# Kernel optimization log

Measured on AMD Instinct MI355X. Metric: run time of the kernel, lower is better.

The kernel has to match this reference:

```python
import jax, jax.numpy as jnp
import numpy as np
from jax import lax

B, L, D_MODEL = 2, 2048, 1024
D_INNER, D_STATE, DT_RANK, D_CONV = 2048, 16, 64, 4


def setup_inputs() -> dict:
    key = jax.random.key(0)
    ks = jax.random.split(key, 10)
    s = 0.02
    A_log = jnp.log(jnp.broadcast_to(jnp.arange(1, D_STATE + 1, dtype=jnp.float32), (D_INNER, D_STATE)))
    return {
        "x": jax.random.normal(ks[0], (B, L, D_MODEL), jnp.float32),
        "in_proj_w": jax.random.normal(ks[1], (2 * D_INNER, D_MODEL), jnp.float32) * s,
        "conv_w": jax.random.normal(ks[2], (D_INNER, 1, D_CONV), jnp.float32) * s,
        "conv_b": jax.random.normal(ks[3], (D_INNER,), jnp.float32) * s,
        "x_proj_w": jax.random.normal(ks[4], (DT_RANK + 2 * D_STATE, D_INNER), jnp.float32) * s,
        "dt_proj_w": jax.random.normal(ks[5], (D_INNER, DT_RANK), jnp.float32) * s,
        "dt_proj_b": jax.random.normal(ks[6], (D_INNER,), jnp.float32) * s,
        "A_log": A_log,
        "D": jnp.ones((D_INNER,), jnp.float32),
        "out_proj_w": jax.random.normal(ks[7], (D_MODEL, D_INNER), jnp.float32) * s,
    }


def _silu(v):
    return v * jax.nn.sigmoid(v)


def _mamba_forward(x, in_proj_w, conv_w, conv_b, x_proj_w, dt_proj_w, dt_proj_b, A_log, D, out_proj_w):
    b, l, _ = x.shape
    xr = jnp.einsum('bld,ed->ble', x, in_proj_w)          # (b, l, 2*d_inner)
    xs, res = jnp.split(xr, 2, axis=-1)
    # causal depthwise conv over time
    xc = jnp.transpose(xs, (0, 2, 1))                     # (b, d_inner, l)
    xc = lax.conv_general_dilated(
        xc, conv_w, window_strides=(1,), padding=[(D_CONV - 1, 0)],
        feature_group_count=D_INNER,
        dimension_numbers=('NCH', 'OIH', 'NCH')) + conv_b[None, :, None]
    u = _silu(jnp.transpose(xc, (0, 2, 1)))               # (b, l, d_inner)
    # SSM parameters
    A = -jnp.exp(A_log)                                   # (d_inner, d_state)
    x_dbl = jnp.einsum('bld,ed->ble', u, x_proj_w)        # (b, l, dt_rank + 2*d_state)
    dt, Bm, Cm = jnp.split(x_dbl, [DT_RANK, DT_RANK + D_STATE], axis=-1)
    delta = jax.nn.softplus(jnp.einsum('blr,dr->bld', dt, dt_proj_w) + dt_proj_b)
    # discretize
    deltaA = jnp.exp(jnp.einsum('bld,dn->bldn', delta, A))        # (b, l, d_inner, d_state)
    deltaBu = jnp.einsum('bld,bln,bld->bldn', delta, Bm, u)       # (b, l, d_inner, d_state)
    # sequential selective scan over time
    def step(h, inp):
        dA, dBu, c = inp
        h = dA * h + dBu                                  # (b, d_inner, d_state)
        y = jnp.einsum('bdn,bn->bd', h, c)
        return h, y
    xs_scan = (jnp.transpose(deltaA, (1, 0, 2, 3)),
               jnp.transpose(deltaBu, (1, 0, 2, 3)),
               jnp.transpose(Cm, (1, 0, 2)))
    h0 = jnp.zeros((b, D_INNER, D_STATE), u.dtype)
    _, ys = lax.scan(step, h0, xs_scan)                   # (l, b, d_inner)
    y = jnp.transpose(ys, (1, 0, 2)) + u * D              # skip connection
    y = y * _silu(res)                                    # gate
    return jnp.einsum('bld,ed->ble', y, out_proj_w)       # (b, l, d_model)


def reference(x, in_proj_w, conv_w, conv_b, x_proj_w, dt_proj_w, dt_proj_b, A_log, D, out_proj_w):
    return _mamba_forward(x, in_proj_w, conv_w, conv_b, x_proj_w, dt_proj_w, dt_proj_b, A_log, D, out_proj_w)
```

## Files before the change

kernel.cpp:

```cpp
#include <hip/hip_runtime.h>
#include <hip/hip_bf16.h>
#include <math.h>

#define B_SZ 2
#define L_SZ 2048
#define DMODEL 1024
#define DINNER 2048
#define DSTATE 16
#define DTRANK 64
#define M_ROWS (B_SZ * L_SZ)

#define CH 32
#define CLEN (L_SZ / CH)
#define CPB 64

#define KSPLIT 8
#define KC (DINNER / KSPLIT)

typedef short shortx8 __attribute__((ext_vector_type(8)));
typedef float floatx4 __attribute__((ext_vector_type(4)));
typedef float floatx16 __attribute__((ext_vector_type(16)));

__device__ __forceinline__ float softplusf(float x) {
    return fmaxf(x, 0.f) + log1pf(expf(-fabsf(x)));
}
__device__ __forceinline__ float siluf(float x) {
    return x * (1.f / (1.f + expf(-x)));
}

__device__ __forceinline__ void async_ld16(const void* g, void* l) {
    __builtin_amdgcn_global_load_lds(
        (__attribute__((address_space(1))) void*)(unsigned long long)g,
        (__attribute__((address_space(3))) void*)(unsigned int)(unsigned long long)l,
        16, 0, 0);
}


template <int ROWS, int KSRC>
__global__ __launch_bounds__(256) void split3_kernel(
    const float* __restrict__ src, unsigned short* __restrict__ dst)
{
    constexpr int SEGT = KSRC / 64;
    int i = blockIdx.x * 256 + threadIdx.x;
    int row = i & (ROWS - 1);
    int k8s = i / ROWS;
    const float* s = src + (size_t)row * KSRC + k8s * 8;
    float4 v0 = *(const float4*)s;
    float4 v1 = *(const float4*)(s + 4);
    float vs[8] = {v0.x, v0.y, v0.z, v0.w, v1.x, v1.y, v1.z, v1.w};
    unsigned short hsv[8], lsv[8];
#pragma unroll
    for (int j = 0; j < 8; ++j) {
        __hip_bfloat16 h = __float2bfloat16(vs[j]);
        __hip_bfloat16 l = __float2bfloat16(vs[j] - __bfloat162float(h));
        hsv[j] = *(unsigned short*)&h;
        lsv[j] = *(unsigned short*)&l;
    }
    int tloc = k8s >> 3;
    int sh = (k8s >> 2) & 1;
    int k8l = k8s & 3;
    size_t off = ((size_t)(row >> 8) * 4 * SEGT + tloc * 2 + sh) * 8192
               + (size_t)(k8l * 256 + (row & 255)) * 8;
    *(shortx8*)&dst[off] = *(shortx8*)hsv;
    *(shortx8*)&dst[off + (size_t)2 * SEGT * 8192] = *(shortx8*)lsv;
}

template <int LDSRC>
__global__ __launch_bounds__(256) void split2k_kernel(
    const float* __restrict__ src, unsigned short* __restrict__ dst)
{
    int i = blockIdx.x * 256 + threadIdx.x;
    int m = i >> 6, k = i & 63;
    float a = src[(size_t)m * LDSRC + k];
    __hip_bfloat16 h = __float2bfloat16(a);
    __hip_bfloat16 l = __float2bfloat16(a - __bfloat162float(h));
    unsigned short* row = dst + (size_t)m * 128;
    row[k] = *(unsigned short*)&h;
    row[64 + k] = *(unsigned short*)&l;
}

template <int KT, int SEGT, int NB, int LDC>
__global__ __launch_bounds__(512, 2) void gemm_8ph(
    const unsigned short* __restrict__ Ap,
    const unsigned short* __restrict__ Bp,
    float* __restrict__ C)
{
    __shared__ unsigned short lds[65536];

    const int tid = threadIdx.x;
    const int lane = tid & 63;
    const int w = tid >> 6;
    const int wm = w >> 2, wn = w & 3;
    const int l15 = lane & 15, l4 = lane >> 4;

    int id = blockIdx.x;
    id = (id & 7) * 32 + (id >> 3);
    const int bm = id / NB;
    const int bn = id % NB;

    const unsigned short* ga = Ap + (size_t)bm * 4 * SEGT * 8192;
    const unsigned short* gb = Bp + (size_t)bn * 4 * SEGT * 8192;

    const int rA = (l4 * 256 + wm * 128 + l15) * 8;
    const int rB = (l4 * 256 + wn * 64 + l15) * 8;

    floatx4 acc[8][4] = {};
    shortx8 bfr[4];

    auto STAGE = [&](int vt, int ab, int s) {
        int Tv = vt < KT ? vt : KT - 1;
        int Tm = ab ? (Tv >= SEGT ? Tv - SEGT : Tv)
                    : (Tv >= 2 * SEGT ? Tv - 2 * SEGT : Tv);
        const unsigned short* src = (ab ? gb : ga) + ((size_t)Tm * 2 + s) * 8192 + tid * 8;
        unsigned short* dst = (unsigned short*)lds + (vt & 1) * 32768 + ab * 16384 + s * 8192 + tid * 8;
        async_ld16(src, dst);
        async_ld16(src + 4096, dst + 4096);
    };

#define MFMA16(MH)                                                                             \
    acc[(MH)*4+0][0] = __builtin_amdgcn_mfma_f32_16x16x32_bf16(af0, bfr[0], acc[(MH)*4+0][0], 0,0,0); \
    acc[(MH)*4+0][1] = __builtin_amdgcn_mfma_f32_16x16x32_bf16(af0, bfr[1], acc[(MH)*4+0][1], 0,0,0); \
    acc[(MH)*4+0][2] = __builtin_amdgcn_mfma_f32_16x16x32_bf16(af0, bfr[2], acc[(MH)*4+0][2], 0,0,0); \
    acc[(MH)*4+0][3] = __builtin_amdgcn_mfma_f32_16x16x32_bf16(af0, bfr[3], acc[(MH)*4+0][3], 0,0,0); \
    acc[(MH)*4+1][0] = __builtin_amdgcn_mfma_f32_16x16x32_bf16(af1, bfr[0], acc[(MH)*4+1][0], 0,0,0); \
    acc[(MH)*4+1][1] = __builtin_amdgcn_mfma_f32_16x16x32_bf16(af1, bfr[1], acc[(MH)*4+1][1], 0,0,0); \
    acc[(MH)*4+1][2] = __builtin_amdgcn_mfma_f32_16x16x32_bf16(af1, bfr[2], acc[(MH)*4+1][2], 0,0,0); \
    acc[(MH)*4+1][3] = __builtin_amdgcn_mfma_f32_16x16x32_bf16(af1, bfr[3], acc[(MH)*4+1][3], 0,0,0); \
    acc[(MH)*4+2][0] = __builtin_amdgcn_mfma_f32_16x16x32_bf16(af2, bfr[0], acc[(MH)*4+2][0], 0,0,0); \
    acc[(MH)*4+2][1] = __builtin_amdgcn_mfma_f32_16x16x32_bf16(af2, bfr[1], acc[(MH)*4+2][1], 0,0,0); \
    acc[(MH)*4+2][2] = __builtin_amdgcn_mfma_f32_16x16x32_bf16(af2, bfr[2], acc[(MH)*4+2][2], 0,0,0); \
    acc[(MH)*4+2][3] = __builtin_amdgcn_mfma_f32_16x16x32_bf16(af2, bfr[3], acc[(MH)*4+2][3], 0,0,0); \
    acc[(MH)*4+3][0] = __builtin_amdgcn_mfma_f32_16x16x32_bf16(af3, bfr[0], acc[(MH)*4+3][0], 0,0,0); \
    acc[(MH)*4+3][1] = __builtin_amdgcn_mfma_f32_16x16x32_bf16(af3, bfr[1], acc[(MH)*4+3][1], 0,0,0); \
    acc[(MH)*4+3][2] = __builtin_amdgcn_mfma_f32_16x16x32_bf16(af3, bfr[2], acc[(MH)*4+3][2], 0,0,0); \
    acc[(MH)*4+3][3] = __builtin_amdgcn_mfma_f32_16x16x32_bf16(af3, bfr[3], acc[(MH)*4+3][3], 0,0,0);

#define PHASE(SLOT, S, MH, SVT, SAB, SS, VM)                                   \
    {                                                                          \
        const unsigned short* Ab = &lds[(SLOT)*32768 + (S)*8192] + rA;         \
        shortx8 af0 = *(const shortx8*)&Ab[((MH)*4 + 0) * 128];                \
        shortx8 af1 = *(const shortx8*)&Ab[((MH)*4 + 1) * 128];                \
        shortx8 af2 = *(const shortx8*)&Ab[((MH)*4 + 2) * 128];                \
        shortx8 af3 = *(const shortx8*)&Ab[((MH)*4 + 3) * 128];                \
        if ((MH) == 0) {                                                       \
            const unsigned short* Bb = &lds[(SLOT)*32768 + 16384 + (S)*8192] + rB; \
            bfr[0] = *(const shortx8*)&Bb[0];                                  \
            bfr[1] = *(const shortx8*)&Bb[128];                                \
            bfr[2] = *(const shortx8*)&Bb[256];                                \
            bfr[3] = *(const shortx8*)&Bb[384];                                \
        }                                                                      \
        STAGE(SVT, SAB, SS);                                                   \
        __builtin_amdgcn_s_barrier();                                          \
        asm volatile("s_waitcnt lgkmcnt(0)" ::: "memory");                     \
        __builtin_amdgcn_s_setprio(1);                                         \
        MFMA16(MH)                                                             \
        __builtin_amdgcn_s_setprio(0);                                         \
        if (VM) { asm volatile("s_waitcnt vmcnt(4)" ::: "memory"); }           \
        __builtin_amdgcn_s_barrier();                                          \
    }

    STAGE(0, 0, 0); STAGE(0, 1, 0); STAGE(0, 0, 1); STAGE(0, 1, 1);
    STAGE(1, 0, 0); STAGE(1, 1, 0);
    asm volatile("s_waitcnt vmcnt(4)" ::: "memory");
    __builtin_amdgcn_s_barrier();

#pragma unroll 1
    for (int i = 0; i < KT / 2; ++i) {
        const int t2 = 2 * i;
        PHASE(0, 0, 0, t2 + 1, 0, 1, 0)
        PHASE(0, 0, 1, t2 + 1, 1, 1, 0)
        PHASE(0, 1, 0, t2 + 2, 0, 0, 0)
        PHASE(0, 1, 1, t2 + 2, 1, 0, 1)
        PHASE(1, 0, 0, t2 + 2, 0, 1, 0)
        PHASE(1, 0, 1, t2 + 2, 1, 1, 0)
        PHASE(1, 1, 0, t2 + 3, 0, 0, 0)
        PHASE(1, 1, 1, t2 + 3, 1, 0, 1)
    }

#undef PHASE
#undef MFMA16

    const int c0 = bn * 256 + wn * 64;
    const int r0 = bm * 256 + wm * 128;
#pragma unroll
    for (int fi = 0; fi < 8; ++fi) {
#pragma unroll
        for (int fj = 0; fj < 4; ++fj) {
            int col = c0 + fj * 16 + l15;
            int rowb = r0 + fi * 16 + l4 * 4;
#pragma unroll
            for (int ri = 0; ri < 4; ++ri)
                C[(size_t)(rowb + ri) * LDC + col] = acc[fi][fj][ri];
        }
    }
}

template <int BN, int KP>
__global__ __launch_bounds__(256) void gemm_bf16_nt(
    const unsigned short* __restrict__ A,
    const unsigned short* __restrict__ Bm,
    float* __restrict__ C, int ldc)
{
    constexpr int TN32 = BN / 64;
    __shared__ unsigned short As[2 * 8192];
    __shared__ unsigned short Bs[2 * BN * 64];

    const int tid = threadIdx.x;
    const int w = tid >> 6;
    const int lane = tid & 63;
    const int wm = w >> 1, wn = w & 1;
    const int m0 = blockIdx.y * 128;
    const int n0 = blockIdx.x * BN;

    const int r4 = lane >> 2;
    const int csw = (lane & 3) ^ ((r4 >> 1) & 3);
    const int gk = csw * 8;
    const int l31 = lane & 31;
    const int khalf = lane >> 5;
    const int rsw = (l31 >> 1) & 3;

    floatx16 acc[2][TN32] = {};

    for (int k0 = 0; k0 < KP; k0 += 64) {
#pragma unroll
        for (int seg = 0; seg < 2; ++seg) {
            const unsigned short* Asrc = A + seg * KP;
            const unsigned short* Bsrc = Bm + seg * KP;
#pragma unroll
            for (int t = 0; t < 2; ++t) {
#pragma unroll
                for (int jj = 0; jj < 2; ++jj) {
                    int j = w + jj * 4;
                    async_ld16(Asrc + (size_t)(m0 + j * 16 + r4) * (2 * KP) + k0 + t * 32 + gk,
                               &As[seg * 8192 + t * 4096 + j * 512]);
                }
#pragma unroll
                for (int jj = 0; jj < BN / 64; ++jj) {
                    int j = w + jj * 4;
                    async_ld16(Bsrc + (size_t)(n0 + j * 16 + r4) * (2 * KP) + k0 + t * 32 + gk,
                               &Bs[seg * BN * 64 + t * BN * 32 + j * 512]);
                }
            }
        }
        __syncthreads();

#pragma unroll
        for (int t = 0; t < 2; ++t) {
#pragma unroll
            for (int kk = 0; kk < 2; ++kk) {
                const int pos = ((kk * 2 + khalf) ^ rsw) << 3;
                shortx8 ah[2], al[2], bh[TN32], bl[TN32];
#pragma unroll
                for (int i = 0; i < 2; ++i) {
                    int row = wm * 64 + i * 32 + l31;
                    ah[i] = *(const shortx8*)&As[t * 4096 + row * 32 + pos];
                    al[i] = *(const shortx8*)&As[8192 + t * 4096 + row * 32 + pos];
                }
#pragma unroll
                for (int j = 0; j < TN32; ++j) {
                    int col = wn * (BN / 2) + j * 32 + l31;
                    bh[j] = *(const shortx8*)&Bs[t * BN * 32 + col * 32 + pos];
                    bl[j] = *(const shortx8*)&Bs[BN * 64 + t * BN * 32 + col * 32 + pos];
                }
#pragma unroll
                for (int i = 0; i < 2; ++i)
#pragma unroll
                    for (int j = 0; j < TN32; ++j) {
                        acc[i][j] = __builtin_amdgcn_mfma_f32_32x32x16_bf16(ah[i], bh[j], acc[i][j], 0, 0, 0);
                        acc[i][j] = __builtin_amdgcn_mfma_f32_32x32x16_bf16(ah[i], bl[j], acc[i][j], 0, 0, 0);
                        acc[i][j] = __builtin_amdgcn_mfma_f32_32x32x16_bf16(al[i], bh[j], acc[i][j], 0, 0, 0);
                    }
            }
        }
        __syncthreads();
    }

#pragma unroll
    for (int i = 0; i < 2; ++i) {
#pragma unroll
        for (int j = 0; j < TN32; ++j) {
            int col = n0 + wn * (BN / 2) + j * 32 + l31;
#pragma unroll
            for (int r = 0; r < 16; ++r) {
                int row = m0 + wm * 64 + i * 32 + (r & 3) + 8 * (r >> 2) + 4 * khalf;
                C[(size_t)row * ldc + col] = acc[i][j][r];
            }
        }
    }
}

template <int BN, int KP>
__global__ __launch_bounds__(256) void gemm_bf16_sp(
    const unsigned short* __restrict__ A,
    const unsigned short* __restrict__ Bm,
    float* __restrict__ C, int ldc, const float* __restrict__ bias)
{
    constexpr int TN32 = BN / 64;
    __shared__ unsigned short As[2 * 8192];
    __shared__ unsigned short Bs[2 * BN * 64];

    const int tid = threadIdx.x;
    const int w = tid >> 6;
    const int lane = tid & 63;
    const int wm = w >> 1, wn = w & 1;
    const int m0 = blockIdx.y * 128;
    const int n0 = blockIdx.x * BN;

    const int r4 = lane >> 2;
    const int csw = (lane & 3) ^ ((r4 >> 1) & 3);
    const int gk = csw * 8;
    const int l31 = lane & 31;
    const int khalf = lane >> 5;
    const int rsw = (l31 >> 1) & 3;

    floatx16 acc[2][TN32] = {};

    for (int k0 = 0; k0 < KP; k0 += 64) {
#pragma unroll
        for (int seg = 0; seg < 2; ++seg) {
            const unsigned short* Asrc = A + seg * KP;
            const unsigned short* Bsrc = Bm + seg * KP;
#pragma unroll
            for (int t = 0; t < 2; ++t) {
#pragma unroll
                for (int jj = 0; jj < 2; ++jj) {
                    int j = w + jj * 4;
                    async_ld16(Asrc + (size_t)(m0 + j * 16 + r4) * (2 * KP) + k0 + t * 32 + gk,
                               &As[seg * 8192 + t * 4096 + j * 512]);
                }
#pragma unroll
                for (int jj = 0; jj < BN / 64; ++jj) {
                    int j = w + jj * 4;
                    async_ld16(Bsrc + (size_t)(n0 + j * 16 + r4) * (2 * KP) + k0 + t * 32 + gk,
                               &Bs[seg * BN * 64 + t * BN * 32 + j * 512]);
                }
            }
        }
        __syncthreads();

#pragma unroll
        for (int t = 0; t < 2; ++t) {
#pragma unroll
            for (int kk = 0; kk < 2; ++kk) {
                const int pos = ((kk * 2 + khalf) ^ rsw) << 3;
                shortx8 ah[2], al[2], bh[TN32], bl[TN32];
#pragma unroll
                for (int i = 0; i < 2; ++i) {
                    int row = wm * 64 + i * 32 + l31;
                    ah[i] = *(const shortx8*)&As[t * 4096 + row * 32 + pos];
                    al[i] = *(const shortx8*)&As[8192 + t * 4096 + row * 32 + pos];
                }
#pragma unroll
                for (int j = 0; j < TN32; ++j) {
                    int col = wn * (BN / 2) + j * 32 + l31;
                    bh[j] = *(const shortx8*)&Bs[t * BN * 32 + col * 32 + pos];
                    bl[j] = *(const shortx8*)&Bs[BN * 64 + t * BN * 32 + col * 32 + pos];
                }
#pragma unroll
                for (int i = 0; i < 2; ++i)
#pragma unroll
                    for (int j = 0; j < TN32; ++j) {
                        acc[i][j] = __builtin_amdgcn_mfma_f32_32x32x16_bf16(ah[i], bh[j], acc[i][j], 0, 0, 0);
                        acc[i][j] = __builtin_amdgcn_mfma_f32_32x32x16_bf16(ah[i], bl[j], acc[i][j], 0, 0, 0);
                        acc[i][j] = __builtin_amdgcn_mfma_f32_32x32x16_bf16(al[i], bh[j], acc[i][j], 0, 0, 0);
                    }
            }
        }
        __syncthreads();
    }

#pragma unroll
    for (int i = 0; i < 2; ++i) {
#pragma unroll
        for (int j = 0; j < TN32; ++j) {
            int col = n0 + wn * (BN / 2) + j * 32 + l31;
            float bz = bias[col];
#pragma unroll
            for (int r = 0; r < 16; ++r) {
                int row = m0 + wm * 64 + i * 32 + (r & 3) + 8 * (r >> 2) + 4 * khalf;
                C[(size_t)row * ldc + col] = softplusf(acc[i][j][r] + bz);
            }
        }
    }
}

__global__ __launch_bounds__(256) void split2_kernel(
    const float* __restrict__ src, unsigned short* __restrict__ dst, int K)
{
    int i = blockIdx.x * 256 + threadIdx.x;
    int m = i / K;
    int k = i - m * K;
    float a = src[i];
    __hip_bfloat16 h = __float2bfloat16(a);
    __hip_bfloat16 l = __float2bfloat16(a - __bfloat162float(h));
    unsigned short* row = dst + (size_t)m * 2 * K;
    row[k] = *(unsigned short*)&h;
    row[K + k] = *(unsigned short*)&l;
}

__global__ __launch_bounds__(256) void xproj_splitk(
    const float* __restrict__ u, const float* __restrict__ Wx,
    float* __restrict__ Cp)
{
    __shared__ float As[64][68];
    __shared__ float Bs[64][100];

    const int tid = threadIdx.x;
    const int ks = blockIdx.x;
    const int m0 = blockIdx.y * 64;
    const int tx = tid & 15;
    const int ty = tid >> 4;

    float acc[4][6] = {};

    for (int k0 = ks * KC; k0 < (ks + 1) * KC; k0 += 64) {
        for (int idx = tid * 4; idx < 64 * 64; idx += 1024) {
            int row = idx >> 6, kk = idx & 63;
            float4 v = *(const float4*)&u[(size_t)(m0 + row) * DINNER + k0 + kk];
            As[kk + 0][row] = v.x;
            As[kk + 1][row] = v.y;
            As[kk + 2][row] = v.z;
            As[kk + 3][row] = v.w;
        }
        for (int idx = tid * 4; idx < 96 * 64; idx += 1024) {
            int row = idx >> 6, kk = idx & 63;
            float4 v = *(const float4*)&Wx[(size_t)row * DINNER + k0 + kk];
            Bs[kk + 0][row] = v.x;
            Bs[kk + 1][row] = v.y;
            Bs[kk + 2][row] = v.z;
            Bs[kk + 3][row] = v.w;
        }
        __syncthreads();

#pragma unroll 8
        for (int k = 0; k < 64; ++k) {
            float a[4], b[6];
#pragma unroll
            for (int i = 0; i < 4; ++i) a[i] = As[k][ty * 4 + i];
#pragma unroll
            for (int j = 0; j < 6; ++j) b[j] = Bs[k][tx * 6 + j];
#pragma unroll
            for (int i = 0; i < 4; ++i)
#pragma unroll
                for (int j = 0; j < 6; ++j) acc[i][j] = fmaf(a[i], b[j], acc[i][j]);
        }
        __syncthreads();
    }

    float* outp = Cp + ((size_t)ks * M_ROWS + m0) * 96;
#pragma unroll
    for (int i = 0; i < 4; ++i)
#pragma unroll
        for (int j = 0; j < 6; ++j)
            outp[(ty * 4 + i) * 96 + tx * 6 + j] = acc[i][j];
}

__global__ __launch_bounds__(256) void xproj_reduce(
    const float* __restrict__ Cp, float* __restrict__ xdbl)
{
    int i = blockIdx.x * 256 + threadIdx.x;
    float s = 0.f;
#pragma unroll
    for (int c = 0; c < KSPLIT; ++c)
        s += Cp[(size_t)c * M_ROWS * 96 + i];
    xdbl[i] = s;
}

__global__ __launch_bounds__(256) void conv_silu_v4(
    const float* __restrict__ xz, const float* __restrict__ cw,
    const float* __restrict__ cb, float* __restrict__ u)
{
    int i = blockIdx.x * 256 + threadIdx.x;
    int dq = (i & 511) << 2;
    int bl = i >> 9;
    int b = bl >> 11;
    int l = bl & 2047;

    float4 W0 = *(const float4*)&cw[(dq + 0) * 4];
    float4 W1 = *(const float4*)&cw[(dq + 1) * 4];
    float4 W2 = *(const float4*)&cw[(dq + 2) * 4];
    float4 W3 = *(const float4*)&cw[(dq + 3) * 4];
    float4 acc = *(const float4*)&cb[dq];

#pragma unroll
    for (int k = 0; k < 4; ++k) {
        int ls = l + k - 3;
        if (ls >= 0) {
            float4 v = *(const float4*)&xz[((size_t)(b << 11) + ls) * 4096 + dq];
            acc.x = fmaf(v.x, ((const float*)&W0)[k], acc.x);
            acc.y = fmaf(v.y, ((const float*)&W1)[k], acc.y);
            acc.z = fmaf(v.z, ((const float*)&W2)[k], acc.z);
            acc.w = fmaf(v.w, ((const float*)&W3)[k], acc.w);
        }
    }
    float4 r = make_float4(siluf(acc.x), siluf(acc.y), siluf(acc.z), siluf(acc.w));
    *(float4*)&u[(size_t)bl * DINNER + dq] = r;
}

template <bool PASS3>
__global__ __launch_bounds__(256) void scan_chunk(
    const float* __restrict__ dbuf, const float* __restrict__ ubuf,
    const float* __restrict__ xdbl, const float* __restrict__ A_log,
    const float* __restrict__ Dv,
    float* __restrict__ Pbuf, float* __restrict__ Sbuf,
    const float* __restrict__ xz, unsigned short* __restrict__ y2)
{
    __shared__ float sd[16][CPB];
    __shared__ float su[16][CPB];
    __shared__ float sB[16][DSTATE];
    __shared__ float sC[16][DSTATE];

    const int tid = threadIdx.x;
    const int c    = blockIdx.x % CH;
    const int dblk = (blockIdx.x / CH) % (DINNER / CPB);
    const int b    = blockIdx.x / (CH * (DINNER / CPB));
    const int d0 = dblk * CPB;
    const int dg = tid >> 2;
    const int q  = tid & 3;
    const int d  = d0 + dg;
    const size_t base_bl = (size_t)b * L_SZ + (size_t)c * CLEN;

    float Ac[4], h[4];
    float sdl = 0.f;
#pragma unroll
    for (int j = 0; j < 4; ++j)
        Ac[j] = -expf(A_log[d * DSTATE + 4 * q + j]);
    const size_t psoff = (((size_t)b * CH + c) * DINNER + d0) * DSTATE + (size_t)tid * 4;
    if (PASS3) {
        float4 h0 = *(const float4*)&Sbuf[psoff];
        h[0] = h0.x; h[1] = h0.y; h[2] = h0.z; h[3] = h0.w;
    } else {
        h[0] = h[1] = h[2] = h[3] = 0.f;
    }
    const float Dd = PASS3 ? Dv[d] : 0.f;

    const int ls = tid >> 4;
    const int g4 = (tid & 15) * 4;
    const int ln = tid & 15;

    float4 r_d = *(const float4*)&dbuf[(base_bl + ls) * DINNER + d0 + g4];
    float4 r_u = *(const float4*)&ubuf[(base_bl + ls) * DINNER + d0 + g4];
    float r_B = xdbl[(base_bl + ls) * 96 + 64 + ln];
    float r_C = xdbl[(base_bl + ls) * 96 + 80 + ln];

    for (int l0 = 0; l0 < CLEN; l0 += 16) {
        __syncthreads();
        *(float4*)&sd[ls][g4] = r_d;
        *(float4*)&su[ls][g4] = r_u;
        sB[ls][ln] = r_B;
        sC[ls][ln] = r_C;
        __syncthreads();

        if (l0 + 16 < CLEN) {
            r_d = *(const float4*)&dbuf[(base_bl + l0 + 16 + ls) * DINNER + d0 + g4];
            r_u = *(const float4*)&ubuf[(base_bl + l0 + 16 + ls) * DINNER + d0 + g4];
            r_B = xdbl[(base_bl + l0 + 16 + ls) * 96 + 64 + ln];
            r_C = xdbl[(base_bl + l0 + 16 + ls) * 96 + 80 + ln];
        }

#pragma unroll
        for (int s = 0; s < 16; ++s) {
            float dl = sd[s][dg];
            float ul = su[s][dg];
            float4 Bv = *(float4*)&sB[s][4 * q];
            float dbu = dl * ul;
            float dA0 = expf(dl * Ac[0]);
            float dA1 = expf(dl * Ac[1]);
            float dA2 = expf(dl * Ac[2]);
            float dA3 = expf(dl * Ac[3]);
            h[0] = fmaf(dA0, h[0], dbu * Bv.x);
            h[1] = fmaf(dA1, h[1], dbu * Bv.y);
            h[2] = fmaf(dA2, h[2], dbu * Bv.z);
            h[3] = fmaf(dA3, h[3], dbu * Bv.w);
            if (!PASS3) {
                sdl += dl;
            } else {
                float4 Cv = *(float4*)&sC[s][4 * q];
                float y = h[0] * Cv.x + h[1] * Cv.y + h[2] * Cv.z + h[3] * Cv.w;
                y += __shfl_xor(y, 1);
                y += __shfl_xor(y, 2);
                if (q == 0) su[s][dg] = fmaf(ul, Dd, y);
            }
        }

        if (PASS3) {
            __syncthreads();
            size_t row = base_bl + l0 + ls;
            float4 yv = *(float4*)&su[ls][g4];
            float4 rv = *(const float4*)&xz[row * 4096 + 2048 + d0 + g4];
            float a0 = yv.x * siluf(rv.x);
            float a1 = yv.y * siluf(rv.y);
            float a2 = yv.z * siluf(rv.z);
            float a3 = yv.w * siluf(rv.w);
            __hip_bfloat16 h0 = __float2bfloat16(a0), h1 = __float2bfloat16(a1);
            __hip_bfloat16 h2 = __float2bfloat16(a2), h3 = __float2bfloat16(a3);
            __hip_bfloat16 l0b = __float2bfloat16(a0 - __bfloat162float(h0));
            __hip_bfloat16 l1b = __float2bfloat16(a1 - __bfloat162float(h1));
            __hip_bfloat16 l2b = __float2bfloat16(a2 - __bfloat162float(h2));
            __hip_bfloat16 l3b = __float2bfloat16(a3 - __bfloat162float(h3));
            ushort4 hv = make_ushort4(*(unsigned short*)&h0, *(unsigned short*)&h1,
                                      *(unsigned short*)&h2, *(unsigned short*)&h3);
            ushort4 lv = make_ushort4(*(unsigned short*)&l0b, *(unsigned short*)&l1b,
                                      *(unsigned short*)&l2b, *(unsigned short*)&l3b);
            unsigned short* yrow = y2 + row * 2 * DINNER + d0 + g4;
            *(ushort4*)&yrow[0] = hv;
            *(ushort4*)&yrow[DINNER] = lv;
        }
    }

    if (!PASS3) {
        *(float4*)&Pbuf[psoff] = make_float4(expf(Ac[0] * sdl), expf(Ac[1] * sdl),
                                             expf(Ac[2] * sdl), expf(Ac[3] * sdl));
        *(float4*)&Sbuf[psoff] = make_float4(h[0], h[1], h[2], h[3]);
    }
}

__global__ __launch_bounds__(256) void scan_combine(
    const float* __restrict__ Pbuf, float* __restrict__ Sbuf)
{
    int t = blockIdx.x * 256 + threadIdx.x;
    int b = t >> 15;
    int rem = t & 32767;
    size_t base = (size_t)b * CH * DINNER * DSTATE + rem;
    float H = 0.f;
#pragma unroll 4
    for (int c = 0; c < CH; ++c) {
        size_t off = base + (size_t)c * DINNER * DSTATE;
        float S = Sbuf[off];
        float P = Pbuf[off];
        Sbuf[off] = H;
        H = fmaf(P, H, S);
    }
}

extern "C" void kernel_launch(void* const* d_in, const int* in_sizes, int n_in,
                              void* d_out, int out_size, void* d_ws, size_t ws_size,
                              hipStream_t stream)
{
    const float* x          = (const float*)d_in[0];
    const float* in_proj_w  = (const float*)d_in[1];
    const float* conv_w     = (const float*)d_in[2];
    const float* conv_b     = (const float*)d_in[3];
    const float* x_proj_w   = (const float*)d_in[4];
    const float* dt_proj_w  = (const float*)d_in[5];
    const float* dt_proj_b  = (const float*)d_in[6];
    const float* A_log      = (const float*)d_in[7];
    const float* Dv         = (const float*)d_in[8];
    const float* out_proj_w = (const float*)d_in[9];
    float* out = (float*)d_out;

    char* w = (char*)d_ws;
    float* xz   = (float*)(w);
    float* u    = (float*)(w + 67108864);
    float* dbuf = (float*)(w + 100663296);
    float* xdbl = (float*)(w + 134217728);
    float* Pbuf = (float*)(w + 135790592);
    float* Sbuf = (float*)(w + 144179200);
    unsigned short* y2  = (unsigned short*)(w + 152567808);
    unsigned short* w2b = (unsigned short*)(w + 135790592);
    float* Cp = (float*)(w + 152567808);
    unsigned short* dt2  = (unsigned short*)(w + 152567808);
    unsigned short* wdt2 = (unsigned short*)(w + 152567808 + 1048576);
    unsigned short* x2p  = (unsigned short*)(w + 67108864);
    unsigned short* w2ap = (unsigned short*)(w + 100663296);

    split3_kernel<4096, 1024><<<2048, 256, 0, stream>>>(x, x2p);
    split3_kernel<4096, 1024><<<2048, 256, 0, stream>>>(in_proj_w, w2ap);
    gemm_8ph<48, 16, 16, 4096><<<256, 512, 0, stream>>>(x2p, w2ap, xz);
    conv_silu_v4<<<(M_ROWS * 512) / 256, 256, 0, stream>>>(xz, conv_w, conv_b, u);
    {
        dim3 g(KSPLIT, M_ROWS / 64);
        xproj_splitk<<<g, 256, 0, stream>>>(u, x_proj_w, Cp);
        xproj_reduce<<<(M_ROWS * 96) / 256, 256, 0, stream>>>(Cp, xdbl);
    }
    {
        split2k_kernel<96><<<1024, 256, 0, stream>>>(xdbl, dt2);
        split2k_kernel<64><<<512, 256, 0, stream>>>(dt_proj_w, wdt2);
        dim3 g(DINNER / 64, M_ROWS / 128);
        gemm_bf16_sp<64, 64><<<g, 256, 0, stream>>>(dt2, wdt2, dbuf, DINNER, dt_proj_b);
    }
    {
        const int nblk = B_SZ * (DINNER / CPB) * CH;
        scan_chunk<false><<<nblk, 256, 0, stream>>>(dbuf, u, xdbl, A_log, Dv, Pbuf, Sbuf, nullptr, nullptr);
        scan_combine<<<B_SZ * DINNER * DSTATE / 256, 256, 0, stream>>>(Pbuf, Sbuf);
        scan_chunk<true><<<nblk, 256, 0, stream>>>(dbuf, u, xdbl, A_log, Dv, nullptr, Sbuf, xz, y2);
    }
    split2_kernel<<<(DMODEL * DINNER) / 256, 256, 0, stream>>>(out_proj_w, w2b, DINNER);
    {
        dim3 g(1024 / 64, M_ROWS / 128);
        gemm_bf16_nt<64, 2048><<<g, 256, 0, stream>>>(y2, w2b, out, 1024);
    }
}
```

Baseline: 510.0 us.

## Use 128x128 tiles with 8 waves for out_proj GEMM; coarsen split3 threads

The out_proj bf16x3 GEMM now uses 128x128 output tiles with 512 threads (8 waves, each computing 64x32) in place of 128x64 tiles with 4 waves. This halves the number of times the A operand is reloaded across N tiles and raises the MFMA work per block. The grid shrinks to 8x32 = 256 blocks, which may underfill the CUs. Separately, the split3 conversion kernel has each thread process 32 consecutive floats instead of 8, using a quarter of the blocks. This cuts index math and improves read contiguity.

Measured after the change: 500.4 us. About the same (-1.9%).

```diff
diff --git a/kernel.cpp b/kernel.cpp
--- a/kernel.cpp
+++ b/kernel.cpp
@@ -43,26 +43,29 @@
     constexpr int SEGT = KSRC / 64;
     int i = blockIdx.x * 256 + threadIdx.x;
     int row = i & (ROWS - 1);
-    int k8s = i / ROWS;
-    const float* s = src + (size_t)row * KSRC + k8s * 8;
-    float4 v0 = *(const float4*)s;
-    float4 v1 = *(const float4*)(s + 4);
-    float vs[8] = {v0.x, v0.y, v0.z, v0.w, v1.x, v1.y, v1.z, v1.w};
-    unsigned short hsv[8], lsv[8];
-#pragma unroll
-    for (int j = 0; j < 8; ++j) {
-        __hip_bfloat16 h = __float2bfloat16(vs[j]);
-        __hip_bfloat16 l = __float2bfloat16(vs[j] - __bfloat162float(h));
-        hsv[j] = *(unsigned short*)&h;
-        lsv[j] = *(unsigned short*)&l;
-    }
-    int tloc = k8s >> 3;
-    int sh = (k8s >> 2) & 1;
-    int k8l = k8s & 3;
-    size_t off = ((size_t)(row >> 8) * 4 * SEGT + tloc * 2 + sh) * 8192
-               + (size_t)(k8l * 256 + (row & 255)) * 8;
-    *(shortx8*)&dst[off] = *(shortx8*)hsv;
-    *(shortx8*)&dst[off + (size_t)2 * SEGT * 8192] = *(shortx8*)lsv;
+    int g = i / ROWS;
+    const float* s = src + (size_t)row * KSRC + g * 32;
+    int tloc = g >> 1;
+    int sh = g & 1;
+    size_t base = ((size_t)(row >> 8) * 4 * SEGT + tloc * 2 + sh) * 8192
+                + (size_t)(row & 255) * 8;
+#pragma unroll
+    for (int q = 0; q < 4; ++q) {
+        float4 v0 = *(const float4*)(s + q * 8);
+        float4 v1 = *(const float4*)(s + q * 8 + 4);
+        float fs[8] = {v0.x, v0.y, v0.z, v0.w, v1.x, v1.y, v1.z, v1.w};
+        shortx8 hv, lv;
+#pragma unroll
+        for (int j = 0; j < 8; ++j) {
+            __hip_bfloat16 h = __float2bfloat16(fs[j]);
+            __hip_bfloat16 l = __float2bfloat16(fs[j] - __bfloat162float(h));
+            hv[j] = *(unsigned short*)&h;
+            lv[j] = *(unsigned short*)&l;
+        }
+        size_t off = base + (size_t)q * 2048;
+        *(shortx8*)&dst[off] = hv;
+        *(shortx8*)&dst[off + (size_t)2 * SEGT * 8192] = lv;
+    }
 }
 
 template <int LDSRC>
@@ -195,22 +198,22 @@
     }
 }
 
-template <int BN, int KP>
-__global__ __launch_bounds__(256) void gemm_bf16_nt(
+template <int KP>
+__global__ __launch_bounds__(512) void gemm_bf16_128x128(
     const unsigned short* __restrict__ A,
     const unsigned short* __restrict__ Bm,
     float* __restrict__ C, int ldc)
 {
-    constexpr int TN32 = BN / 64;
     __shared__ unsigned short As[2 * 8192];
-    __shared__ unsigned short Bs[2 * BN * 64];
+    __shared__ unsigned short Bs[2 * 8192];
 
     const int tid = threadIdx.x;
     const int w = tid >> 6;
     const int lane = tid & 63;
-    const int wm = w >> 1, wn = w & 1;
+    const int wm = w >> 2;
+    const int wn = w & 3;
     const int m0 = blockIdx.y * 128;
-    const int n0 = blockIdx.x * BN;
+    const int n0 = blockIdx.x * 128;
 
     const int r4 = lane >> 2;
     const int csw = (lane & 3) ^ ((r4 >> 1) & 3);
@@ -219,7 +222,7 @@
     const int khalf = lane >> 5;
     const int rsw = (l31 >> 1) & 3;
 
-    floatx16 acc[2][TN32] = {};
+    floatx16 acc[2] = {};
 
     for (int k0 = 0; k0 < KP; k0 += 64) {
 #pragma unroll
@@ -228,18 +231,10 @@
             const unsigned short* Bsrc = Bm + seg * KP;
 #pragma unroll
             for (int t = 0; t < 2; ++t) {
-#pragma unroll
-                for (int jj = 0; jj < 2; ++jj) {
-                    int j = w + jj * 4;
-                    async_ld16(Asrc + (size_t)(m0 + j * 16 + r4) * (2 * KP) + k0 + t * 32 + gk,
-                               &As[seg * 8192 + t * 4096 + j * 512]);
-                }
-#pragma unroll
-                for (int jj = 0; jj < BN / 64; ++jj) {
-                    int j = w + jj * 4;
-                    async_ld16(Bsrc + (size_t)(n0 + j * 16 + r4) * (2 * KP) + k0 + t * 32 + gk,
-                               &Bs[seg * BN * 64 + t * BN * 32 + j * 512]);
-                }
+                async_ld16(Asrc + (size_t)(m0 + w * 16 + r4) * (2 * KP) + k0 + t * 32 + gk,
+                           &As[seg * 8192 + t * 4096 + w * 512]);
+                async_ld16(Bsrc + (size_t)(n0 + w * 16 + r4) * (2 * KP) + k0 + t * 32 + gk,
+                           &Bs[seg * 8192 + t * 4096 + w * 512]);
             }
         }
         __syncthreads();
@@ -249,27 +244,24 @@
 #pragma unroll
             for (int kk = 0; kk < 2; ++kk) {
                 const int pos = ((kk * 2 + khalf) ^ rsw) << 3;
-                shortx8 ah[2], al[2], bh[TN32], bl[TN32];
+                shortx8 ah[2], al[2], bh, bl;
 #pragma unroll
                 for (int i = 0; i < 2; ++i) {
                     int row = wm * 64 + i * 32 + l31;
                     ah[i] = *(const shortx8*)&As[t * 4096 + row * 32 + pos];
                     al[i] = *(const shortx8*)&As[8192 + t * 4096 + row * 32 + pos];
                 }
-#pragma unroll
-                for (int j = 0; j < TN32; ++j) {
-                    int col = wn * (BN / 2) + j * 32 + l31;
-                    bh[j] = *(const shortx8*)&Bs[t * BN * 32 + col * 32 + pos];
-                    bl[j] = *(const shortx8*)&Bs[BN * 64 + t * BN * 32 + col * 32 + pos];
+                {
+                    int col = wn * 32 + l31;
+                    bh = *(const shortx8*)&Bs[t * 4096 + col * 32 + pos];
+                    bl = *(const shortx8*)&Bs[8192 + t * 4096 + col * 32 + pos];
                 }
 #pragma unroll
-                for (int i = 0; i < 2; ++i)
-#pragma unroll
-                    for (int j = 0; j < TN32; ++j) {
-                        acc[i][j] = __builtin_amdgcn_mfma_f32_32x32x16_bf16(ah[i], bh[j], acc[i][j], 0, 0, 0);
-                        acc[i][j] = __builtin_amdgcn_mfma_f32_32x32x16_bf16(ah[i], bl[j], acc[i][j], 0, 0, 0);
-                        acc[i][j] = __builtin_amdgcn_mfma_f32_32x32x16_bf16(al[i], bh[j], acc[i][j], 0, 0, 0);
-                    }
+                for (int i = 0; i < 2; ++i) {
+                    acc[i] = __builtin_amdgcn_mfma_f32_32x32x16_bf16(ah[i], bh, acc[i], 0, 0, 0);
+                    acc[i] = __builtin_amdgcn_mfma_f32_32x32x16_bf16(ah[i], bl, acc[i], 0, 0, 0);
+                    acc[i] = __builtin_amdgcn_mfma_f32_32x32x16_bf16(al[i], bh, acc[i], 0, 0, 0);
+                }
             }
         }
         __syncthreads();
@@ -277,14 +269,11 @@
 
 #pragma unroll
     for (int i = 0; i < 2; ++i) {
-#pragma unroll
-        for (int j = 0; j < TN32; ++j) {
-            int col = n0 + wn * (BN / 2) + j * 32 + l31;
-#pragma unroll
-            for (int r = 0; r < 16; ++r) {
-                int row = m0 + wm * 64 + i * 32 + (r & 3) + 8 * (r >> 2) + 4 * khalf;
-                C[(size_t)row * ldc + col] = acc[i][j][r];
-            }
+        int col = n0 + wn * 32 + l31;
+#pragma unroll
+        for (int r = 0; r < 16; ++r) {
+            int row = m0 + wm * 64 + i * 32 + (r & 3) + 8 * (r >> 2) + 4 * khalf;
+            C[(size_t)row * ldc + col] = acc[i][r];
         }
     }
 }
@@ -664,8 +653,8 @@
     unsigned short* x2p  = (unsigned short*)(w + 67108864);
     unsigned short* w2ap = (unsigned short*)(w + 100663296);
 
-    split3_kernel<4096, 1024><<<2048, 256, 0, stream>>>(x, x2p);
-    split3_kernel<4096, 1024><<<2048, 256, 0, stream>>>(in_proj_w, w2ap);
+    split3_kernel<4096, 1024><<<512, 256, 0, stream>>>(x, x2p);
+    split3_kernel<4096, 1024><<<512, 256, 0, stream>>>(in_proj_w, w2ap);
     gemm_8ph<48, 16, 16, 4096><<<256, 512, 0, stream>>>(x2p, w2ap, xz);
     conv_silu_v4<<<(M_ROWS * 512) / 256, 256, 0, stream>>>(xz, conv_w, conv_b, u);
     {
@@ -687,7 +676,7 @@
     }
     split2_kernel<<<(DMODEL * DINNER) / 256, 256, 0, stream>>>(out_proj_w, w2b, DINNER);
     {
-        dim3 g(1024 / 64, M_ROWS / 128);
-        gemm_bf16_nt<64, 2048><<<g, 256, 0, stream>>>(y2, w2b, out, 1024);
-    }
-}
+        dim3 g(DMODEL / 128, M_ROWS / 128);
+        gemm_bf16_128x128<2048><<<g, 512, 0, stream>>>(y2, w2b, out, 1024);
+    }
+}
```
